# Kernel optimization log

Measured on AMD Instinct MI355X. Metric: run time of the kernel, lower is better.

The kernel has to match this reference:

```python
import jax, jax.numpy as jnp
import numpy as np

K_H = 2  # matches init_kwargs k_h
K_W = 2  # matches init_kwargs k_w


def setup_inputs() -> dict:
    key = jax.random.key(0)
    k1, k2, k3 = jax.random.split(key, 3)
    B, C, H, W = 8, 128, 128, 128
    inp = jax.random.normal(k1, (B, C, H, W), dtype=jnp.float32)
    offset_x = jax.random.normal(k2, (B, 1, H * K_H, W * K_W), dtype=jnp.float32)
    offset_y = jax.random.normal(k3, (B, 1, H * K_H, W * K_W), dtype=jnp.float32)
    return {"input": inp, "offset_x": offset_x, "offset_y": offset_y}


def _bilinear_sample(img, y, x):
    # img: [C, H, W]; y, x: [Ho, Wo] float sampling coordinates (input-pixel units)
    C, H, W = img.shape
    y0f = jnp.floor(y)
    x0f = jnp.floor(x)
    wy = y - y0f  # fractional weights, [Ho, Wo]
    wx = x - x0f
    y0 = y0f.astype(jnp.int32)
    x0 = x0f.astype(jnp.int32)

    def gather(yi, xi):
        # zero-padded gather outside the image (deformable-conv style)
        valid = (yi >= 0) & (yi < H) & (xi >= 0) & (xi < W)
        v = img[:, jnp.clip(yi, 0, H - 1), jnp.clip(xi, 0, W - 1)]  # [C, Ho, Wo]
        return jnp.where(valid[None], v, jnp.zeros((), img.dtype))

    v00 = gather(y0, x0)
    v01 = gather(y0, x0 + 1)
    v10 = gather(y0 + 1, x0)
    v11 = gather(y0 + 1, x0 + 1)
    wy = wy[None]  # [1, Ho, Wo]
    wx = wx[None]
    return (v00 * (1.0 - wy) * (1.0 - wx)
            + v01 * (1.0 - wy) * wx
            + v10 * wy * (1.0 - wx)
            + v11 * wy * wx)


def reference(input, offset_x, offset_y):
    # Location-aware Upsampling: out[b,c,i,j] = bilinear(input[b,c],
    #   y = i/k_h + offset_y[b,0,i,j], x = j/k_w + offset_x[b,0,i,j])
    B, C, H, W = input.shape
    Ho, Wo = H * K_H, W * K_W
    base_y = (jnp.arange(Ho, dtype=input.dtype) / K_H)[:, None]  # [Ho, 1]
    base_x = (jnp.arange(Wo, dtype=input.dtype) / K_W)[None, :]  # [1, Wo]
    y = base_y + offset_y[:, 0]  # [B, Ho, Wo]
    x = base_x + offset_x[:, 0]  # [B, Ho, Wo]
    return jax.vmap(_bilinear_sample)(input, y, x)  # [B, C, Ho, Wo]
```

## Files before the change

kernel.cpp:

```cpp
#include <hip/hip_runtime.h>


constexpr int B  = 8;
constexpr int C  = 128;
constexpr int H  = 128;
constexpr int W  = 128;
constexpr int KH = 2;
constexpr int KW = 2;
constexpr int Ho = H * KH;
constexpr int Wo = W * KW;
constexpr int HW = H * W;
constexpr int CG  = 4;
constexpr int CPG = C / CG;
constexpr int NC  = 2;
constexpr int NSTAGE = CPG / NC;
constexpr int TR = 16;
constexpr int ADV = TR / 2;
constexpr int WR = 16;
constexpr int WWORDS = WR * W;
constexpr int NXT = Ho / TR;

using f32x4 = __attribute__((ext_vector_type(4))) float;

__global__ __launch_bounds__(1024, 8) void deform_upsample_kernel(
    const float* __restrict__ in,
    const float* __restrict__ offx,
    const float* __restrict__ offy,
    float* __restrict__ out)
{
    __shared__ float smem[2][NC * WWORDS];

    const int wgid  = blockIdx.x;
    const int xcd   = wgid & 7;
    const int k     = wgid >> 3;
    const int bx    = k & (NXT - 1);
    const int slice = xcd * 4 + (k >> 4);
    const int bz    = slice & (CG - 1);
    const int b     = slice >> 2;

    const int t    = threadIdx.x;
    const int lane = t & 63;
    const int wv   = t >> 6;
    const int wo4  = lane * 4;
    const int ho   = bx * TR + wv;
    const int c0   = bz * CPG;

    const int iy0 = min(max(bx * ADV - 4, 0), H - WR);

    const int fw  = t * 4;
    const int chs = fw >> 11;
    const int rem = fw & (WWORDS - 1);
    const float* gsrc = in + (size_t)(b * C + c0 + chs) * HW + iy0 * W + rem;

    float4 stg = *reinterpret_cast<const float4*>(gsrc);

    const int sbase = (b * Ho + ho) * Wo + wo4;
    const float4 ox4 = *reinterpret_cast<const float4*>(offx + sbase);
    const float4 oy4 = *reinterpret_cast<const float4*>(offy + sbase);
    const float oxv[4] = {ox4.x, ox4.y, ox4.z, ox4.w};
    const float oyv[4] = {oy4.x, oy4.y, oy4.z, oy4.w};

    float wt0[4], wt1[4], wb0[4], wb1[4];
    int   otv[4], obv[4];
    unsigned fbmask = 0;

    const float base_y = (float)ho * 0.5f;
#pragma unroll
    for (int j = 0; j < 4; ++j) {
        const float y = base_y + oyv[j];
        const float x = (float)(wo4 + j) * 0.5f + oxv[j];
        const float y0f = floorf(y), x0f = floorf(x);
        const float wy = y - y0f, wx = x - x0f;
        const int y0 = (int)y0f, x0 = (int)x0f;
        const int y1 = y0 + 1, x1 = x0 + 1;
        const bool vy0 = ((unsigned)y0 < (unsigned)H);
        const bool vy1 = ((unsigned)y1 < (unsigned)H);
        const bool vx0 = ((unsigned)x0 < (unsigned)W);
        const bool vx1 = ((unsigned)x1 < (unsigned)W);
        const int yc0 = min(max(y0, 0), H - 1);
        const int yc1 = min(max(y1, 0), H - 1);
        const int xc0 = min(max(x0, 0), W - 1);
        const int xc1 = min(max(x1, 0), W - 1);
        const int xb  = min(max(x0, 0), W - 2);

        const float omwy = 1.0f - wy, omwx = 1.0f - wx;
        const float w00 = (vy0 && vx0) ? (omwy * omwx) : 0.0f;
        const float w01 = (vy0 && vx1) ? (omwy * wx)   : 0.0f;
        const float w10 = (vy1 && vx0) ? (wy * omwx)   : 0.0f;
        const float w11 = (vy1 && vx1) ? (wy * wx)     : 0.0f;

        wt0[j] = (xc0 == xb ? w00 : 0.0f) + (xc1 == xb ? w01 : 0.0f);
        wt1[j] = (xc0 == xb ? 0.0f : w00) + (xc1 == xb ? 0.0f : w01);
        wb0[j] = (xc0 == xb ? w10 : 0.0f) + (xc1 == xb ? w11 : 0.0f);
        wb1[j] = (xc0 == xb ? 0.0f : w10) + (xc1 == xb ? 0.0f : w11);

        const int yr0 = yc0 - iy0, yr1 = yc1 - iy0;
        fbmask |= (unsigned)((yr0 < 0) | (yr1 > WR - 1)) << j;
        const int yr0c = min(max(yr0, 0), WR - 1);
        const int yr1c = min(max(yr1, 0), WR - 1);
        otv[j] = yr0c * W + xb;
        obv[j] = yr1c * W + xb;
    }

    *reinterpret_cast<float4*>(&smem[0][fw]) = stg;
    gsrc += NC * HW;
    stg = *reinterpret_cast<const float4*>(gsrc);
    __syncthreads();

    const float* ipfb = in + (size_t)(b * C + c0) * HW;
    float* op = out + ((size_t)(b * C + c0) * Ho + ho) * Wo + wo4;

    int cur = 0;
    for (int s = 0; s < NSTAGE; ++s) {
#pragma unroll
        for (int c = 0; c < NC; ++c) {
            const float* lw = &smem[cur][c * WWORDS];
            float r[4];
#pragma unroll
            for (int j = 0; j < 4; ++j) {
                const float t0v = lw[otv[j]];
                const float t1v = lw[otv[j] + 1];
                const float b0v = lw[obv[j]];
                const float b1v = lw[obv[j] + 1];
                float acc = wt0[j] * t0v;
                acc = fmaf(wt1[j], t1v, acc);
                acc = fmaf(wb0[j], b0v, acc);
                acc = fmaf(wb1[j], b1v, acc);
                r[j] = acc;
            }
            if (__builtin_expect(fbmask != 0u, 0)) {
                const float* ipc = ipfb + (size_t)(s * NC + c) * HW;
#pragma unroll
                for (int j = 0; j < 4; ++j) {
                    if ((fbmask >> j) & 1u) {
                        const float y = base_y + oyv[j];
                        const int y0 = (int)floorf(y);
                        const int yc0 = min(max(y0, 0), H - 1);
                        const int yc1 = min(max(y0 + 1, 0), H - 1);
                        const int xb  = otv[j] & (W - 1);
                        const float t0v = ipc[yc0 * W + xb];
                        const float t1v = ipc[yc0 * W + xb + 1];
                        const float b0v = ipc[yc1 * W + xb];
                        const float b1v = ipc[yc1 * W + xb + 1];
                        float acc = wt0[j] * t0v;
                        acc = fmaf(wt1[j], t1v, acc);
                        acc = fmaf(wb0[j], b0v, acc);
                        acc = fmaf(wb1[j], b1v, acc);
                        r[j] = acc;
                    }
                }
            }
            f32x4 rv = {r[0], r[1], r[2], r[3]};
            __builtin_nontemporal_store(
                rv, reinterpret_cast<f32x4*>(op + (size_t)(s * NC + c) * (size_t)(Ho * Wo)));
        }
        __syncthreads();
        if (s + 1 < NSTAGE) {
            *reinterpret_cast<float4*>(&smem[cur ^ 1][fw]) = stg;
            if (s + 2 < NSTAGE) {
                gsrc += NC * HW;
                stg = *reinterpret_cast<const float4*>(gsrc);
            }
            __syncthreads();
            cur ^= 1;
        }
    }
}

extern "C" void kernel_launch(void* const* d_in, const int* in_sizes, int n_in,
                              void* d_out, int out_size, void* d_ws, size_t ws_size,
                              hipStream_t stream) {
    const float* in   = (const float*)d_in[0];
    const float* offx = (const float*)d_in[1];
    const float* offy = (const float*)d_in[2];
    float* out = (float*)d_out;

    dim3 grid(NXT * B * CG);
    dim3 block(1024);
    deform_upsample_kernel<<<grid, block, 0, stream>>>(in, offx, offy, out);
}
```

Baseline: 321.5 us.

## Stage four channels per pass and drop one barrier per stage

Doubles the channels staged in LDS per pipeline step from two to four, so each thread now prefetches two float4 rows. The pipeline is restructured: at the start of each stage the next buffer is written and the following loads are issued, then the current buffer is consumed, leaving a single LDS-only barrier per stage. The reuse is safe because the barrier at the end of the previous stage guarantees all waves finished reading that buffer. The fallback path now reloads offy from global memory instead of keeping it in registers, to relieve register pressure. LDS use per block doubles to 64 KB, which may limit how many blocks fit on a CU.

```diff
diff --git a/kernel.cpp b/kernel.cpp
--- a/kernel.cpp
+++ b/kernel.cpp
@@ -12,15 +12,21 @@
 constexpr int HW = H * W;
 constexpr int CG  = 4;
 constexpr int CPG = C / CG;
-constexpr int NC  = 2;
+constexpr int NC  = 4;
 constexpr int NSTAGE = CPG / NC;
 constexpr int TR = 16;
 constexpr int ADV = TR / 2;
 constexpr int WR = 16;
 constexpr int WWORDS = WR * W;
+constexpr int PACK = NC * WWORDS;
 constexpr int NXT = Ho / TR;
 
 using f32x4 = __attribute__((ext_vector_type(4))) float;
+
+__device__ inline void lds_barrier() {
+    asm volatile("s_waitcnt lgkmcnt(0)" ::: "memory");
+    __builtin_amdgcn_s_barrier();
+}
 
 __global__ __launch_bounds__(1024, 8) void deform_upsample_kernel(
     const float* __restrict__ in,
@@ -28,7 +34,7 @@
     const float* __restrict__ offy,
     float* __restrict__ out)
 {
-    __shared__ float smem[2][NC * WWORDS];
+    __shared__ float smem[2][PACK];
 
     const int wgid  = blockIdx.x;
     const int xcd   = wgid & 7;
@@ -47,12 +53,15 @@
 
     const int iy0 = min(max(bx * ADV - 4, 0), H - WR);
 
-    const int fw  = t * 4;
-    const int chs = fw >> 11;
-    const int rem = fw & (WWORDS - 1);
-    const float* gsrc = in + (size_t)(b * C + c0 + chs) * HW + iy0 * W + rem;
+    const int fw0 = t * 4;
+    const int fw1 = t * 4 + 4096;
+    const float* gsrcA = in + (size_t)(b * C + c0 + (fw0 >> 11)) * HW
+                            + iy0 * W + (fw0 & (WWORDS - 1));
+    const float* gsrcB = in + (size_t)(b * C + c0 + (fw1 >> 11)) * HW
+                            + iy0 * W + (fw1 & (WWORDS - 1));
 
-    float4 stg = *reinterpret_cast<const float4*>(gsrc);
+    float4 stgA = *reinterpret_cast<const float4*>(gsrcA);
+    float4 stgB = *reinterpret_cast<const float4*>(gsrcB);
 
     const int sbase = (b * Ho + ho) * Wo + wo4;
     const float4 ox4 = *reinterpret_cast<const float4*>(offx + sbase);
@@ -102,16 +111,29 @@
         obv[j] = yr1c * W + xb;
     }
 
-    *reinterpret_cast<float4*>(&smem[0][fw]) = stg;
-    gsrc += NC * HW;
-    stg = *reinterpret_cast<const float4*>(gsrc);
-    __syncthreads();
+    *reinterpret_cast<float4*>(&smem[0][fw0]) = stgA;
+    *reinterpret_cast<float4*>(&smem[0][fw1]) = stgB;
+    gsrcA += NC * HW;  gsrcB += NC * HW;
+    stgA = *reinterpret_cast<const float4*>(gsrcA);
+    stgB = *reinterpret_cast<const float4*>(gsrcB);
+    lds_barrier();
 
     const float* ipfb = in + (size_t)(b * C + c0) * HW;
     float* op = out + ((size_t)(b * C + c0) * Ho + ho) * Wo + wo4;
 
-    int cur = 0;
     for (int s = 0; s < NSTAGE; ++s) {
+        const int cur = s & 1;
+
+        if (s + 1 < NSTAGE) {
+            *reinterpret_cast<float4*>(&smem[cur ^ 1][fw0]) = stgA;
+            *reinterpret_cast<float4*>(&smem[cur ^ 1][fw1]) = stgB;
+            if (s + 2 < NSTAGE) {
+                gsrcA += NC * HW;  gsrcB += NC * HW;
+                stgA = *reinterpret_cast<const float4*>(gsrcA);
+                stgB = *reinterpret_cast<const float4*>(gsrcB);
+            }
+        }
+
 #pragma unroll
         for (int c = 0; c < NC; ++c) {
             const float* lw = &smem[cur][c * WWORDS];
@@ -133,7 +155,8 @@
 #pragma unroll
                 for (int j = 0; j < 4; ++j) {
                     if ((fbmask >> j) & 1u) {
-                        const float y = base_y + oyv[j];
+                        const float oyj = offy[sbase + j];
+                        const float y = base_y + oyj;
                         const int y0 = (int)floorf(y);
                         const int yc0 = min(max(y0, 0), H - 1);
                         const int yc1 = min(max(y0 + 1, 0), H - 1);
@@ -154,16 +177,9 @@
             __builtin_nontemporal_store(
                 rv, reinterpret_cast<f32x4*>(op + (size_t)(s * NC + c) * (size_t)(Ho * Wo)));
         }
-        __syncthreads();
-        if (s + 1 < NSTAGE) {
-            *reinterpret_cast<float4*>(&smem[cur ^ 1][fw]) = stg;
-            if (s + 2 < NSTAGE) {
-                gsrc += NC * HW;
-                stg = *reinterpret_cast<const float4*>(gsrc);
-            }
-            __syncthreads();
-            cur ^= 1;
-        }
+
+        if (s + 1 < NSTAGE)
+            lds_barrier();
     }
 }
 
```

Result: slower. 334.7 us (+4.1%).
